# Optimization experiments

Measured on AMD Instinct MI355X. Metric: run time of the kernel, lower is better.

The kernel has to match this reference:

```python
import jax, jax.numpy as jnp
import numpy as np

D = 1024          # d_model
EXPAND = 2
DI = EXPAND * D   # d_inner = 2048
K = 4             # d_conv
B, L = 4, 2048
EPS = 1e-6


def setup_inputs() -> dict:
    key = jax.random.key(0)
    ks = jax.random.split(key, 16)
    n = lambda i, shape, scale=0.02: (jax.random.normal(ks[i], shape, jnp.float32) * scale)
    return {
        "x": jax.random.normal(ks[0], (B, L, D), jnp.float32),
        "norm_w": jnp.ones((D,), jnp.float32),
        "up_w": n(1, (D, DI)), "up_b": jnp.zeros((DI,), jnp.float32),
        "gate_w": n(2, (D, DI)), "gate_b": jnp.zeros((DI,), jnp.float32),
        "down_w": n(3, (DI, D)), "down_b": jnp.zeros((D,), jnp.float32),
        "conv_w": n(4, (DI, K), 0.2), "conv_b": jnp.zeros((DI,), jnp.float32),
        "wq": n(5, (D, D)), "wk": n(6, (D, D)), "wv": n(7, (D, D)), "wo": n(8, (D, D)),
        "decay": jnp.float32(0.99),
    }


def _rmsnorm(x, w):
    return x * jax.lax.rsqrt(jnp.mean(x * x, axis=-1, keepdims=True) + EPS) * w


def _forward(x, norm_w, up_w, up_b, gate_w, gate_b, down_w, down_b,
             conv_w, conv_b, wq, wk, wv, wo, decay):
    normed = _rmsnorm(x, norm_w)                              # [B,L,D]
    h = normed @ up_w + up_b                                  # [B,L,DI]
    # causal depthwise conv1d: left-pad K-1, groups = DI
    di = conv_w.shape[0]
    kern = conv_w.T[:, None, :]                               # [K,1,DI] (WIO)
    h = jax.lax.conv_general_dilated(
        h, kern, window_strides=(1,), padding=[(conv_w.shape[1] - 1, 0)],
        dimension_numbers=("NWC", "WIO", "NWC"), feature_group_count=di)
    h = jax.nn.silu(h + conv_b)                               # [B,L,DI]
    # gated MLP combine + down-projection
    out = (h * jax.nn.silu(normed @ gate_w + gate_b)) @ down_w + down_b  # [B,L,D]
    # Hebbian associative memory: M_t = decay*M_{t-1} + k_t^T v_t; y_t = q_t M_t
    q = out @ wq; k = out @ wk; v = out @ wv                  # [B,L,D]
    M0 = jnp.zeros((out.shape[0], out.shape[-1], out.shape[-1]), out.dtype)

    def step(M, qkv):
        qt, kt, vt = qkv                                      # each [B,D]
        M = decay * M + jnp.einsum("bd,be->bde", kt, vt)
        return M, jnp.einsum("bd,bde->be", qt, M)

    _, ys = jax.lax.scan(step, M0, (q.swapaxes(0, 1), k.swapaxes(0, 1), v.swapaxes(0, 1)))
    mem_out = ys.swapaxes(0, 1) @ wo                          # [B,L,D]
    return x + mem_out


def reference(x, norm_w, up_w, up_b, gate_w, gate_b, down_w, down_b,
              conv_w, conv_b, wq, wk, wv, wo, decay):
    return _forward(x, norm_w, up_w, up_b, gate_w, gate_b, down_w, down_b,
                    conv_w, conv_b, wq, wk, wv, wo, decay)
```

## Files before the change

### kernel.cpp

```cpp
#include <hip/hip_runtime.h>


typedef __bf16 bf16x8 __attribute__((ext_vector_type(8)));
typedef unsigned short u16x8 __attribute__((ext_vector_type(8)));
typedef float f32x4 __attribute__((ext_vector_type(4)));

constexpr int Bb = 4, Ll = 2048, Dd = 1024, DIc = 2048;
constexpr long LD  = (long)Ll * Dd;
constexpr long BLD = (long)Bb * LD;

static __device__ __forceinline__ unsigned short f2bf(float f) {
  unsigned u = __builtin_bit_cast(unsigned, f);
  u += 0x7fffu + ((u >> 16) & 1u);
  return (unsigned short)(u >> 16);
}
static __device__ __forceinline__ float bf2f(unsigned short u) {
  return __builtin_bit_cast(float, (unsigned)u << 16);
}
static __device__ __forceinline__ float silu(float g) {
  return g / (1.f + __expf(-g));
}

enum { EP_UG = 0, EP_DOWN, EP_GV, EP_DECAY, EP_YO };

#define STAGE_A(DBUF, MG, KH, TILE) {                                          \
    const int kt_ = ((TILE) < NTm1 ? (TILE) : NTm1);                           \
    __builtin_amdgcn_global_load_lds(                                          \
      (const __attribute__((address_space(1))) void*)                          \
        (Ag + (size_t)(aRow + (MG)*64) * lda + kt_*64 + (KH)*32 + aCol),       \
      (__attribute__((address_space(3))) void*)                                \
        (lds + (DBUF)*ADB + (KH)*AKH + (aRb + (MG)*4)*512), 16, 0, 0); }

#define STAGE_B(DBUF, NH, KH, TILE) {                                          \
    const int kt_ = ((TILE) < NTm1 ? (TILE) : NTm1);                           \
    __builtin_amdgcn_global_load_lds(                                          \
      (const __attribute__((address_space(1))) void*)                          \
        (Bg + (size_t)(bRow + (NH)*128) * ldb + kt_*64 + (KH)*32 + aCol),      \
      (__attribute__((address_space(3))) void*)                                \
        (lds + BOFF + (DBUF)*16384 + (KH)*8192 + ((NH)*8 + w)*512), 16, 0, 0); }

#define LOAD_A(DBUF, KS, MG) {                                                 \
  _Pragma("unroll") for (int j_ = 0; j_ < 4; ++j_)                             \
    af[j_] = *(const bf16x8*)&lds[(DBUF)*ADB + (KS)*AKH +                      \
        (aRdBase + (MG)*4 + j_)*512 + fr*32 + cph]; }

#define LOAD_B(DBUF, KS) {                                                     \
  _Pragma("unroll") for (int n_ = 0; n_ < 4; ++n_)                             \
    bfr[KS][n_] = *(const bf16x8*)&lds[BOFF + (DBUF)*16384 + (KS)*8192 +       \
        (bRb + n_)*512 + fr*32 + cph]; }

#define MFMA_PH(KS, MG) {                                                      \
  __builtin_amdgcn_s_setprio(1);                                               \
  _Pragma("unroll") for (int j_ = 0; j_ < 4; ++j_)                             \
  _Pragma("unroll") for (int n_ = 0; n_ < 4; ++n_)                             \
    acc[(MG)*4 + j_][n_] = __builtin_amdgcn_mfma_f32_16x16x32_bf16(            \
        af[j_], bfr[KS][n_], acc[(MG)*4 + j_][n_], 0, 0, 0);                   \
  __builtin_amdgcn_s_setprio(0); }

#define BAR() __builtin_amdgcn_s_barrier()
#define WAIT_LGKM0() { asm volatile("s_waitcnt lgkmcnt(0)" ::: "memory");      \
                       __builtin_amdgcn_sched_barrier(0); }
#define WAIT_LGKM8() asm volatile("s_waitcnt lgkmcnt(8)" ::: "memory")
#define WAIT_VM(N) asm volatile("s_waitcnt vmcnt(" #N ")" ::: "memory")

template <int EPI, int BM>
__global__ __launch_bounds__(512, 2) void gemm8_k(
    const ushort* __restrict__ A, const ushort* __restrict__ Bm,
    void* __restrict__ O0, const float* __restrict__ bias,
    const float* __restrict__ bias2, const float* __restrict__ xres,
    const float* __restrict__ decayp,
    int K, int lda, int ldb, int ldc,
    long sA, long sB, long sC,
    void* __restrict__ O1) {
  constexpr int MF = BM / 32;
  constexpr int ADB = BM * 64;
  constexpr int AKH = BM * 32;
  constexpr int BOFF = BM * 128;
  __shared__ ushort lds[BM == 256 ? 65536 : 49152];

  const int z = blockIdx.z;
  const int gx = gridDim.x;
  const int nwg = gx * gridDim.y;
  const int id = blockIdx.y * gx + blockIdx.x;
  const int chunk = nwg >> 3;
  const int swz = (id & 7) * chunk + (id >> 3);
  const int m0 = (swz / gx) * BM;
  const int n0 = (swz % gx) * 256;

  const int t = threadIdx.x;
  const int lane = t & 63;
  const int w = t >> 6;

  if constexpr (EPI == EP_DECAY) {
    if (n0 > m0) return;
  }
  const ushort* Ag = A + (size_t)z * sA + (size_t)m0 * lda;
  const ushort* Bg = Bm + (size_t)z * sB + (size_t)n0 * ldb;

  int Kend = K;
  if constexpr (EPI == EP_YO) Kend = (K < m0 + BM) ? K : m0 + BM;
  const int NT = Kend >> 6;
  const int NTm1 = NT - 1;
  const int NI = NT >> 1;

  const int lp = lane ^ (((lane >> 5) & 1) << 1);
  const int aCol = (lp & 3) * 8;
  const int bRow = (w >> 2) * 64 + (w & 3) * 16 + (lp >> 2);
  int aRow, aRb, aRdBase;
  if constexpr (BM == 256) {
    aRow = (w >> 2) * 128 + (w & 3) * 16 + (lp >> 2);
    aRb = (w >> 2) * 8 + (w & 3);
    aRdBase = (w >> 2) * 8;
  } else {
    aRow = w * 16 + (lp >> 2);
    aRb = w;
    aRdBase = (w >> 2) * 4;
  }
  const int fr = lane & 15;
  const int kg = (lane >> 4) * 8;
  const int cph = kg ^ (((fr >> 3) & 1) << 4);
  const int bRb = ((w & 3) >> 1) * 8 + ((w & 3) & 1) * 4;

  f32x4 acc[MF][4] = {};
  bf16x8 af[4], bfr[2][4];

  if constexpr (BM == 256) {
    STAGE_A(0, 0, 0, 0); STAGE_A(0, 0, 1, 0); STAGE_A(0, 1, 0, 0); STAGE_A(0, 1, 1, 0);
    STAGE_B(0, 0, 0, 0); STAGE_B(0, 0, 1, 0); STAGE_B(0, 1, 0, 0); STAGE_B(0, 1, 1, 0);
    STAGE_B(1, 0, 0, 1); STAGE_B(1, 0, 1, 1); STAGE_B(1, 1, 0, 1); STAGE_B(1, 1, 1, 1);
    STAGE_A(1, 0, 0, 1); STAGE_A(1, 0, 1, 1);
    WAIT_VM(6);
    BAR();
    for (int i = 0; i < NI; ++i) {
      const int tt = 2 * i;
      LOAD_B(0, 0); LOAD_B(0, 1); LOAD_A(0, 0, 0);
      STAGE_A(1, 1, 0, tt + 1); STAGE_A(1, 1, 1, tt + 1);
      WAIT_LGKM8();
      BAR(); WAIT_LGKM0();
      MFMA_PH(0, 0);
      BAR();
      LOAD_A(0, 0, 1);
      STAGE_B(0, 0, 0, tt + 2); STAGE_B(0, 1, 0, tt + 2);
      BAR(); WAIT_LGKM0();
      MFMA_PH(0, 1);
      BAR();
      LOAD_A(0, 1, 0);
      STAGE_B(0, 0, 1, tt + 2); STAGE_B(0, 1, 1, tt + 2);
      BAR(); WAIT_LGKM0();
      MFMA_PH(1, 0);
      BAR();
      LOAD_A(0, 1, 1);
      STAGE_A(0, 0, 0, tt + 2); STAGE_A(0, 0, 1, tt + 2);
      WAIT_VM(6);
      BAR(); WAIT_LGKM0();
      MFMA_PH(1, 1);
      BAR();
      LOAD_B(1, 0); LOAD_B(1, 1); LOAD_A(1, 0, 0);
      STAGE_A(0, 1, 0, tt + 2); STAGE_A(0, 1, 1, tt + 2);
      WAIT_LGKM8();
      BAR(); WAIT_LGKM0();
      MFMA_PH(0, 0);
      BAR();
      LOAD_A(1, 0, 1);
      STAGE_B(1, 0, 0, tt + 3); STAGE_B(1, 1, 0, tt + 3);
      BAR(); WAIT_LGKM0();
      MFMA_PH(0, 1);
      BAR();
      LOAD_A(1, 1, 0);
      STAGE_B(1, 0, 1, tt + 3); STAGE_B(1, 1, 1, tt + 3);
      BAR(); WAIT_LGKM0();
      MFMA_PH(1, 0);
      BAR();
      LOAD_A(1, 1, 1);
      STAGE_A(1, 0, 0, tt + 3); STAGE_A(1, 0, 1, tt + 3);
      WAIT_VM(6);
      BAR(); WAIT_LGKM0();
      MFMA_PH(1, 1);
      BAR();
    }
  } else {
    STAGE_A(0, 0, 0, 0); STAGE_A(0, 0, 1, 0);
    STAGE_B(0, 0, 0, 0); STAGE_B(0, 1, 0, 0); STAGE_B(0, 0, 1, 0); STAGE_B(0, 1, 1, 0);
    STAGE_B(1, 0, 0, 1); STAGE_B(1, 1, 0, 1); STAGE_B(1, 0, 1, 1); STAGE_B(1, 1, 1, 1);
    WAIT_VM(4);
    BAR();
    for (int i = 0; i < NI; ++i) {
      const int tt = 2 * i;
      LOAD_B(0, 0); LOAD_B(0, 1); LOAD_A(0, 0, 0);
      STAGE_A(1, 0, 0, tt + 1); STAGE_A(1, 0, 1, tt + 1);
      WAIT_LGKM8();
      BAR(); WAIT_LGKM0();
      MFMA_PH(0, 0);
      BAR();
      LOAD_A(0, 1, 0);
      STAGE_B(0, 0, 0, tt + 2); STAGE_B(0, 1, 0, tt + 2);
      STAGE_B(0, 0, 1, tt + 2); STAGE_B(0, 1, 1, tt + 2);
      WAIT_VM(4);
      BAR(); WAIT_LGKM0();
      MFMA_PH(1, 0);
      BAR();
      LOAD_B(1, 0); LOAD_B(1, 1); LOAD_A(1, 0, 0);
      STAGE_A(0, 0, 0, tt + 2); STAGE_A(0, 0, 1, tt + 2);
      WAIT_LGKM8();
      BAR(); WAIT_LGKM0();
      MFMA_PH(0, 0);
      BAR();
      LOAD_A(1, 1, 0);
      STAGE_B(1, 0, 0, tt + 3); STAGE_B(1, 1, 0, tt + 3);
      STAGE_B(1, 0, 1, tt + 3); STAGE_B(1, 1, 1, tt + 3);
      WAIT_VM(4);
      BAR(); WAIT_LGKM0();
      MFMA_PH(1, 0);
      BAR();
    }
  }

  const int rb4 = (lane >> 4) * 4;
  const int wm = (w >> 2) * (BM / 2), wn = (w & 3) * 64;
  float logd = 0.f;
  if constexpr (EPI == EP_DECAY) logd = __logf(decayp[0]);

#pragma unroll
  for (int mf = 0; mf < MF; ++mf) {
#pragma unroll
    for (int nf = 0; nf < 4; ++nf) {
      const int gm0 = m0 + wm + mf * 16 + rb4;
      const int gn = n0 + wn + nf * 16 + fr;
      if constexpr (EPI == EP_GV) {
        if (gn < 1024) {
#pragma unroll
          for (int r = 0; r < 4; ++r)
            ((ushort*)O0)[(size_t)(gm0 + r) * 1024 + gn] = f2bf(acc[mf][nf][r]);
        } else {
          const int d = gn - 1024, b = gm0 >> 11, ttp = gm0 & 2047;
          ushort4 w4;
          w4.x = f2bf(acc[mf][nf][0]); w4.y = f2bf(acc[mf][nf][1]);
          w4.z = f2bf(acc[mf][nf][2]); w4.w = f2bf(acc[mf][nf][3]);
          *(ushort4*)&((ushort*)O1)[(size_t)b * LD + (size_t)d * Ll + ttp] = w4;
        }
      } else {
#pragma unroll
        for (int r = 0; r < 4; ++r) {
          const int gm = gm0 + r;
          const size_t idx = (size_t)z * sC + (size_t)gm * ldc + gn;
          const float v = acc[mf][nf][r];
          if constexpr (EPI == EP_UG) {
            const float b = (gn < 2048) ? bias[gn] : bias2[gn - 2048];
            ((ushort*)O0)[idx] = f2bf(v + b);
          } else if constexpr (EPI == EP_DOWN) {
            ((ushort*)O0)[idx] = f2bf(v + bias[gn]);
          } else if constexpr (EPI == EP_DECAY) {
            ((ushort*)O0)[idx] =
                (gn <= gm) ? f2bf(v * __expf((float)(gm - gn) * logd)) : (ushort)0;
          } else {
            ((float*)O0)[idx] = v + xres[idx];
          }
        }
      }
    }
  }
}

__global__ __launch_bounds__(256) void prep_k(
    const float* __restrict__ up_w, const float* __restrict__ gate_w,
    const float* __restrict__ down_w, const float* __restrict__ wq,
    const float* __restrict__ wk, const float* __restrict__ wv,
    const float* __restrict__ wo, const float* __restrict__ conv_w,
    const float* __restrict__ x, const float* __restrict__ norm_w,
    ushort* __restrict__ ugw, ushort* __restrict__ down_wT,
    ushort* __restrict__ wq_bf, ushort* __restrict__ wk_bf,
    ushort* __restrict__ wv_bf, ushort* __restrict__ wo_T,
    ushort* __restrict__ cwT, ushort* __restrict__ nrm) {
  const int bid = blockIdx.x;
  const int t = threadIdx.x;
  if (bid < 7168) {
    const float* src; ushort* dst; int R, C, idx;
    if (bid < 2048)      { src = up_w;   dst = ugw;               R = 1024; C = 2048; idx = bid; }
    else if (bid < 4096) { src = gate_w; dst = ugw + 2048 * 1024; R = 1024; C = 2048; idx = bid - 2048; }
    else if (bid < 6144) { src = down_w; dst = down_wT;           R = 2048; C = 1024; idx = bid - 4096; }
    else                 { src = wo;     dst = wo_T;              R = 1024; C = 1024; idx = bid - 6144; }
    __shared__ float tile[32][33];
    const int tx = t & 31, ty = t >> 5;
    const int tilesx = C >> 5;
    const int c0 = (idx % tilesx) * 32, r0 = (idx / tilesx) * 32;
#pragma unroll
    for (int i = 0; i < 4; ++i)
      tile[ty + i * 8][tx] = src[(size_t)(r0 + ty + i * 8) * C + c0 + tx];
    __syncthreads();
#pragma unroll
    for (int i = 0; i < 4; ++i)
      dst[(size_t)(c0 + ty + i * 8) * R + r0 + tx] = f2bf(tile[tx][ty + i * 8]);
  } else if (bid < 10240) {
    const int seg = (bid - 7168) >> 10;
    const int idx = (bid - 7168) & 1023;
    const float* src = (seg == 0) ? wq : (seg == 1) ? wk : wv;
    ushort* dst = (seg == 0) ? wq_bf : (seg == 1) ? wk_bf : wv_bf;
    const size_t e = (size_t)idx * 1024 + t * 4;
    const float4 v = *(const float4*)(src + e);
    ushort4 r;
    r.x = f2bf(v.x); r.y = f2bf(v.y); r.z = f2bf(v.z); r.w = f2bf(v.w);
    *(ushort4*)(dst + e) = r;
  } else if (bid < 10248) {
    const int c = (bid - 10240) * 256 + t;
    const float4 v = *(const float4*)(conv_w + c * 4);
    cwT[0 * DIc + c] = f2bf(v.x);
    cwT[1 * DIc + c] = f2bf(v.y);
    cwT[2 * DIc + c] = f2bf(v.z);
    cwT[3 * DIc + c] = f2bf(v.w);
  } else {
    const int row = bid - 10248;
    const float* xr = x + (size_t)row * Dd;
    const float4 v = *(const float4*)(xr + t * 4);
    float ss = v.x * v.x + v.y * v.y + v.z * v.z + v.w * v.w;
#pragma unroll
    for (int m = 32; m; m >>= 1) ss += __shfl_xor(ss, m);
    __shared__ float red[4];
    if ((t & 63) == 0) red[t >> 6] = ss;
    __syncthreads();
    const float total = red[0] + red[1] + red[2] + red[3];
    const float rs = rsqrtf(total * (1.f / (float)Dd) + 1e-6f);
    const float4 wt = *(const float4*)(norm_w + t * 4);
    ushort4 r;
    r.x = f2bf(v.x * rs * wt.x); r.y = f2bf(v.y * rs * wt.y);
    r.z = f2bf(v.z * rs * wt.z); r.w = f2bf(v.w * rs * wt.w);
    *(ushort4*)(nrm + (size_t)row * Dd + t * 4) = r;
  }
}

__global__ __launch_bounds__(256) void conv_gate_k(
    const ushort* __restrict__ ug, const ushort* __restrict__ cwT,
    const float* __restrict__ cb, ushort* __restrict__ o,
    const ushort* __restrict__ wk_bf, const ushort* __restrict__ wq_bf,
    const ushort* __restrict__ wo_T, const ushort* __restrict__ wv_bf,
    ushort* __restrict__ WsT, ushort* __restrict__ Wv2T) {
  const int bid = blockIdx.x;
  const int t = threadIdx.x;
  if (bid < 128) {
    __shared__ ushort lds[8192];
    ushort* As = lds;
    ushort* Bs = lds + 4096;
    const int oo = bid >> 6, lid = bid & 63;
    const int m0 = (lid >> 3) * 128, n0 = (lid & 7) * 128;
    const ushort* A = (oo ? wo_T : wk_bf) + (size_t)m0 * 1024;
    const ushort* B = (oo ? wv_bf : wq_bf) + (size_t)n0 * 1024;
    ushort* C = oo ? Wv2T : WsT;
    const int lane = t & 63, wave = t >> 6;
    const int wm = (wave >> 1) * 64, wn = (wave & 1) * 64;
    const int fr = lane & 15, kg = (lane >> 4) * 8;
    const int srow0 = wave * 16 + (lane >> 2), scol = (lane & 3) * 8;
    f32x4 acc[4][4] = {};
    for (int k0 = 0; k0 < 1024; k0 += 32) {
#pragma unroll
      for (int p = 0; p < 2; ++p) {
        __builtin_amdgcn_global_load_lds(
            (const __attribute__((address_space(1))) void*)
                (A + (size_t)(srow0 + p * 64) * 1024 + k0 + scol),
            (__attribute__((address_space(3))) void*)(As + (p * 4 + wave) * 512),
            16, 0, 0);
        __builtin_amdgcn_global_load_lds(
            (const __attribute__((address_space(1))) void*)
                (B + (size_t)(srow0 + p * 64) * 1024 + k0 + scol),
            (__attribute__((address_space(3))) void*)(Bs + (p * 4 + wave) * 512),
            16, 0, 0);
      }
      __syncthreads();
      bf16x8 af[4], bv[4];
#pragma unroll
      for (int i = 0; i < 4; ++i) {
        af[i] = *(const bf16x8*)&As[(wm + i * 16 + fr) * 32 + kg];
        bv[i] = *(const bf16x8*)&Bs[(wn + i * 16 + fr) * 32 + kg];
      }
#pragma unroll
      for (int mi = 0; mi < 4; ++mi)
#pragma unroll
        for (int ni = 0; ni < 4; ++ni)
          acc[mi][ni] = __builtin_amdgcn_mfma_f32_16x16x32_bf16(
              af[mi], bv[ni], acc[mi][ni], 0, 0, 0);
      __syncthreads();
    }
    const int rb = (lane >> 4) * 4;
#pragma unroll
    for (int mi = 0; mi < 4; ++mi)
#pragma unroll
      for (int ni = 0; ni < 4; ++ni)
#pragma unroll
        for (int r = 0; r < 4; ++r)
          C[(size_t)(m0 + wm + mi * 16 + rb + r) * 1024 + n0 + wn + ni * 16 + fr] =
              f2bf(acc[mi][ni][r]);
    return;
  }

  const int cbid = bid - 128;
  const int cg = t & 31;
  const int ts = t >> 5;
  const int cblk = cbid & 7;
  const int rblk = cbid >> 3;
  const int c = cblk * 256 + cg * 8;
  const int row0 = rblk * 64 + ts * 8;

  u16x8 w[4];
#pragma unroll
  for (int k = 0; k < 4; ++k) w[k] = *(const u16x8*)&cwT[k * DIc + c];
  float wb[8];
  *(float4*)&wb[0] = *(const float4*)(cb + c);
  *(float4*)&wb[4] = *(const float4*)(cb + c + 4);

  u16x8 h3, h2, h1;
  if ((row0 & (Ll - 1)) == 0) {
    h3 = (u16x8){}; h2 = (u16x8){}; h1 = (u16x8){};
  } else {
    h3 = *(const u16x8*)&ug[(size_t)(row0 - 3) * 4096 + c];
    h2 = *(const u16x8*)&ug[(size_t)(row0 - 2) * 4096 + c];
    h1 = *(const u16x8*)&ug[(size_t)(row0 - 1) * 4096 + c];
  }

#pragma unroll
  for (int i = 0; i < 8; ++i) {
    const size_t rbase = (size_t)(row0 + i) * 4096;
    const u16x8 h0 = *(const u16x8*)&ug[rbase + c];
    const u16x8 g  = *(const u16x8*)&ug[rbase + 2048 + c];
    u16x8 ov;
#pragma unroll
    for (int j = 0; j < 8; ++j) {
      float acc = wb[j];
      acc += bf2f(w[0][j]) * bf2f(h3[j]);
      acc += bf2f(w[1][j]) * bf2f(h2[j]);
      acc += bf2f(w[2][j]) * bf2f(h1[j]);
      acc += bf2f(w[3][j]) * bf2f(h0[j]);
      ov[j] = f2bf(silu(acc) * silu(bf2f(g[j])));
    }
    *(u16x8*)&o[(size_t)(row0 + i) * DIc + c] = ov;
    h3 = h2; h2 = h1; h1 = h0;
  }
}

extern "C" void kernel_launch(void* const* d_in, const int* in_sizes, int n_in,
                              void* d_out, int out_size, void* d_ws,
                              size_t ws_size, hipStream_t stream) {
  const float* x      = (const float*)d_in[0];
  const float* norm_w = (const float*)d_in[1];
  const float* up_w   = (const float*)d_in[2];
  const float* up_b   = (const float*)d_in[3];
  const float* gate_w = (const float*)d_in[4];
  const float* gate_b = (const float*)d_in[5];
  const float* down_w = (const float*)d_in[6];
  const float* down_b = (const float*)d_in[7];
  const float* conv_w = (const float*)d_in[8];
  const float* conv_b = (const float*)d_in[9];
  const float* wq     = (const float*)d_in[10];
  const float* wk     = (const float*)d_in[11];
  const float* wv     = (const float*)d_in[12];
  const float* wo     = (const float*)d_in[13];
  const float* decay  = (const float*)d_in[14];
  float* out = (float*)d_out;
  char* w8 = (char*)d_ws;

  const size_t MiB = 1u << 20;
  ushort* nrm      = (ushort*)(w8 + 0 * MiB);
  ushort* ug       = (ushort*)(w8 + 16 * MiB);
  ushort* S        = (ushort*)(w8 + 16 * MiB);
  ushort* combined = (ushort*)(w8 + 80 * MiB);
  ushort* G        = (ushort*)(w8 + 112 * MiB);
  ushort* vT       = (ushort*)(w8 + 144 * MiB);
  ushort* ugw      = (ushort*)(w8 + 176 * MiB);
  ushort* down_wT  = (ushort*)(w8 + 184 * MiB);
  ushort* wq_bf    = (ushort*)(w8 + 188 * MiB);
  ushort* wk_bf    = (ushort*)(w8 + 190 * MiB);
  ushort* wv_bf    = (ushort*)(w8 + 192 * MiB);
  ushort* wo_T     = (ushort*)(w8 + 194 * MiB);
  ushort* WsT      = (ushort*)(w8 + 196 * MiB);
  ushort* Wv2T     = (ushort*)(w8 + 198 * MiB);
  ushort* cwT      = (ushort*)(w8 + 200 * MiB);

  prep_k<<<18440, 256, 0, stream>>>(up_w, gate_w, down_w, wq, wk, wv, wo,
                                    conv_w, x, norm_w,
                                    ugw, down_wT, wq_bf, wk_bf, wv_bf, wo_T,
                                    cwT, nrm);

  gemm8_k<EP_UG, 256><<<dim3(16, 32), 512, 0, stream>>>(
      nrm, ugw, ug, up_b, gate_b, nullptr, nullptr,
      1024, 1024, 1024, 4096, 0, 0, 0, nullptr);

  conv_gate_k<<<1152, 256, 0, stream>>>(ug, cwT, conv_b, combined,
                                        wk_bf, wq_bf, wo_T, wv_bf, WsT, Wv2T);

  gemm8_k<EP_DOWN, 128><<<dim3(4, 64), 512, 0, stream>>>(
      combined, down_wT, nrm, down_b, nullptr, nullptr, nullptr,
      2048, 2048, 2048, 1024, 0, 0, 0, nullptr);

  gemm8_k<EP_GV, 128><<<dim3(8, 64), 512, 0, stream>>>(
      nrm, WsT, G, nullptr, nullptr, nullptr, nullptr,
      1024, 1024, 1024, 1024, 0, 0, 0, vT);

  gemm8_k<EP_DECAY, 256><<<dim3(8, 8, Bb), 512, 0, stream>>>(
      G, nrm, S, nullptr, nullptr, nullptr, decay,
      1024, 1024, 1024, 2048, LD, LD, (long)Ll * Ll, nullptr);

  gemm8_k<EP_YO, 128><<<dim3(4, 16, Bb), 512, 0, stream>>>(
      S, vT, out, nullptr, nullptr, x, nullptr,
      2048, 2048, 2048, 1024, (long)Ll * Ll, LD, LD, nullptr);
}
```

Baseline: 280.5 us.

## Add 128x128 GEMM kernel for causal decay and output GEMMs with balanced scheduling

Adds a new 256-thread 128x128-tile GEMM kernel, which now runs the causal decay-score GEMM and the output GEMM that was previously done by the 512-thread 256/128-row kernel. With finer tiles the triangular masking skips more of the zero upper-triangle work. The output GEMM pairs short and long causal row tiles so workgroups get balanced K lengths. The GV GEMM also switches to 256-row tiles. More, smaller workgroups reduce operand reuse per tile.

```diff
diff --git a/kernel.cpp b/kernel.cpp
--- a/kernel.cpp
+++ b/kernel.cpp
@@ -67,8 +67,7 @@
 __global__ __launch_bounds__(512, 2) void gemm8_k(
     const ushort* __restrict__ A, const ushort* __restrict__ Bm,
     void* __restrict__ O0, const float* __restrict__ bias,
-    const float* __restrict__ bias2, const float* __restrict__ xres,
-    const float* __restrict__ decayp,
+    const float* __restrict__ bias2,
     int K, int lda, int ldb, int ldc,
     long sA, long sB, long sC,
     void* __restrict__ O1) {
@@ -91,15 +90,10 @@
   const int lane = t & 63;
   const int w = t >> 6;
 
-  if constexpr (EPI == EP_DECAY) {
-    if (n0 > m0) return;
-  }
   const ushort* Ag = A + (size_t)z * sA + (size_t)m0 * lda;
   const ushort* Bg = Bm + (size_t)z * sB + (size_t)n0 * ldb;
 
-  int Kend = K;
-  if constexpr (EPI == EP_YO) Kend = (K < m0 + BM) ? K : m0 + BM;
-  const int NT = Kend >> 6;
+  const int NT = K >> 6;
   const int NTm1 = NT - 1;
   const int NI = NT >> 1;
 
@@ -217,8 +211,6 @@
 
   const int rb4 = (lane >> 4) * 4;
   const int wm = (w >> 2) * (BM / 2), wn = (w & 3) * 64;
-  float logd = 0.f;
-  if constexpr (EPI == EP_DECAY) logd = __logf(decayp[0]);
 
 #pragma unroll
   for (int mf = 0; mf < MF; ++mf) {
@@ -247,14 +239,164 @@
           if constexpr (EPI == EP_UG) {
             const float b = (gn < 2048) ? bias[gn] : bias2[gn - 2048];
             ((ushort*)O0)[idx] = f2bf(v + b);
-          } else if constexpr (EPI == EP_DOWN) {
+          } else {
             ((ushort*)O0)[idx] = f2bf(v + bias[gn]);
-          } else if constexpr (EPI == EP_DECAY) {
-            ((ushort*)O0)[idx] =
-                (gn <= gm) ? f2bf(v * __expf((float)(gm - gn) * logd)) : (ushort)0;
-          } else {
-            ((float*)O0)[idx] = v + xres[idx];
           }
+        }
+      }
+    }
+  }
+}
+
+#define S4A(DBUF, MG, KH, TILE) {                                              \
+    const int kt_ = ((TILE) < NTm1 ? (TILE) : NTm1);                           \
+    __builtin_amdgcn_global_load_lds(                                          \
+      (const __attribute__((address_space(1))) void*)                          \
+        (Ag + (size_t)(sRow + (MG)*64) * lda + kt_*64 + (KH)*32 + sCol),       \
+      (__attribute__((address_space(3))) void*)                                \
+        (lds + (DBUF)*8192 + (KH)*4096 + ((MG)*4 + w4)*512), 16, 0, 0); }
+
+#define S4B(DBUF, NH, KH, TILE) {                                              \
+    const int kt_ = ((TILE) < NTm1 ? (TILE) : NTm1);                           \
+    __builtin_amdgcn_global_load_lds(                                          \
+      (const __attribute__((address_space(1))) void*)                          \
+        (Bg + (size_t)(sRow + (NH)*64) * ldb + kt_*64 + (KH)*32 + sCol),       \
+      (__attribute__((address_space(3))) void*)                                \
+        (lds + 16384 + (DBUF)*8192 + (KH)*4096 + ((NH)*4 + w4)*512), 16, 0, 0); }
+
+#define L4A(DBUF, KS) {                                                        \
+  _Pragma("unroll") for (int j_ = 0; j_ < 4; ++j_)                             \
+    af[j_] = *(const bf16x8*)&lds[(DBUF)*8192 + (KS)*4096 +                    \
+        (aRd + j_)*512 + fr*32 + cph]; }
+
+#define L4B(DBUF, KS) {                                                        \
+  _Pragma("unroll") for (int n_ = 0; n_ < 4; ++n_)                             \
+    bfr[KS][n_] = *(const bf16x8*)&lds[16384 + (DBUF)*8192 + (KS)*4096 +       \
+        (bRd + n_)*512 + fr*32 + cph]; }
+
+#define MFMA4(KS) {                                                            \
+  __builtin_amdgcn_s_setprio(1);                                               \
+  _Pragma("unroll") for (int j_ = 0; j_ < 4; ++j_)                             \
+  _Pragma("unroll") for (int n_ = 0; n_ < 4; ++n_)                             \
+    acc[j_][n_] = __builtin_amdgcn_mfma_f32_16x16x32_bf16(                     \
+        af[j_], bfr[KS][n_], acc[j_][n_], 0, 0, 0);                            \
+  __builtin_amdgcn_s_setprio(0); }
+
+template <int EPI>
+__global__ __launch_bounds__(256, 2) void gemm4_k(
+    const ushort* __restrict__ A, const ushort* __restrict__ Bm,
+    void* __restrict__ O0, const float* __restrict__ xres,
+    const float* __restrict__ decayp,
+    int K, int lda, int ldb, int ldc, long sA, long sB, long sC) {
+  __shared__ ushort lds[32768];
+
+  const int t = threadIdx.x;
+  const int lane = t & 63;
+  const int w4 = t >> 6;
+
+  int z, m0, n0;
+  if constexpr (EPI == EP_YO) {
+    const int id = blockIdx.y * gridDim.x + blockIdx.x;
+    const int half = id >> 8;
+    const int u = id & 255;
+    const int nt = u & 7;
+    const int rem = u >> 3;
+    z = rem >> 3;
+    const int i8 = rem & 7;
+    const int mt = half ? (15 - i8) : i8;
+    m0 = mt * 128;
+    n0 = nt * 128;
+  } else {
+    z = blockIdx.z;
+    const int gx = gridDim.x;
+    const int nwg = gx * gridDim.y;
+    const int id = blockIdx.y * gx + blockIdx.x;
+    const int chunk = nwg >> 3;
+    const int swz = (id & 7) * chunk + (id >> 3);
+    m0 = (swz / gx) * 128;
+    n0 = (swz % gx) * 128;
+    if (n0 > m0) return;
+  }
+
+  const ushort* Ag = A + (size_t)z * sA + (size_t)m0 * lda;
+  const ushort* Bg = Bm + (size_t)z * sB + (size_t)n0 * ldb;
+
+  int Kend = K;
+  if constexpr (EPI == EP_YO) Kend = m0 + 128;
+  const int NT = Kend >> 6;
+  const int NTm1 = NT - 1;
+  const int NI = NT >> 1;
+
+  const int lp = lane ^ (((lane >> 5) & 1) << 1);
+  const int sRow = w4 * 16 + (lp >> 2);
+  const int sCol = (lp & 3) * 8;
+  const int fr = lane & 15;
+  const int kg = (lane >> 4) * 8;
+  const int cph = kg ^ (((fr >> 3) & 1) << 4);
+  const int aRd = (w4 >> 1) * 4;
+  const int bRd = (w4 & 1) * 4;
+
+  f32x4 acc[4][4] = {};
+  bf16x8 af[4], bfr[2][4];
+
+  S4A(0, 0, 0, 0); S4A(0, 1, 0, 0); S4A(0, 0, 1, 0); S4A(0, 1, 1, 0);
+  S4B(0, 0, 0, 0); S4B(0, 1, 0, 0); S4B(0, 0, 1, 0); S4B(0, 1, 1, 0);
+  S4B(1, 0, 0, 1); S4B(1, 1, 0, 1); S4B(1, 0, 1, 1); S4B(1, 1, 1, 1);
+  WAIT_VM(4);
+  BAR();
+  for (int i = 0; i < NI; ++i) {
+    const int tt = 2 * i;
+    L4B(0, 0); L4B(0, 1); L4A(0, 0);
+    S4A(1, 0, 0, tt + 1); S4A(1, 1, 0, tt + 1);
+    S4A(1, 0, 1, tt + 1); S4A(1, 1, 1, tt + 1);
+    WAIT_LGKM8();
+    BAR(); WAIT_LGKM0();
+    MFMA4(0);
+    BAR();
+    L4A(0, 1);
+    S4B(0, 0, 0, tt + 2); S4B(0, 1, 0, tt + 2);
+    S4B(0, 0, 1, tt + 2); S4B(0, 1, 1, tt + 2);
+    WAIT_VM(4);
+    BAR(); WAIT_LGKM0();
+    MFMA4(1);
+    BAR();
+    L4B(1, 0); L4B(1, 1); L4A(1, 0);
+    S4A(0, 0, 0, tt + 2); S4A(0, 1, 0, tt + 2);
+    S4A(0, 0, 1, tt + 2); S4A(0, 1, 1, tt + 2);
+    WAIT_LGKM8();
+    BAR(); WAIT_LGKM0();
+    MFMA4(0);
+    BAR();
+    L4A(1, 1);
+    S4B(1, 0, 0, tt + 3); S4B(1, 1, 0, tt + 3);
+    S4B(1, 0, 1, tt + 3); S4B(1, 1, 1, tt + 3);
+    WAIT_VM(4);
+    BAR(); WAIT_LGKM0();
+    MFMA4(1);
+    BAR();
+  }
+
+  const int rb4 = (lane >> 4) * 4;
+  const int wm = (w4 >> 1) * 64, wn = (w4 & 1) * 64;
+  float logd = 0.f;
+  if constexpr (EPI == EP_DECAY) logd = __logf(decayp[0]);
+
+#pragma unroll
+  for (int mf = 0; mf < 4; ++mf) {
+#pragma unroll
+    for (int nf = 0; nf < 4; ++nf) {
+      const int gm0 = m0 + wm + mf * 16 + rb4;
+      const int gn = n0 + wn + nf * 16 + fr;
+#pragma unroll
+      for (int r = 0; r < 4; ++r) {
+        const int gm = gm0 + r;
+        const size_t idx = (size_t)z * sC + (size_t)gm * ldc + gn;
+        const float v = acc[mf][nf][r];
+        if constexpr (EPI == EP_DECAY) {
+          ((ushort*)O0)[idx] =
+              (gn <= gm) ? f2bf(v * __expf((float)(gm - gn) * logd)) : (ushort)0;
+        } else {
+          ((float*)O0)[idx] = v + xres[idx];
         }
       }
     }
@@ -478,25 +620,25 @@
                                     cwT, nrm);
 
   gemm8_k<EP_UG, 256><<<dim3(16, 32), 512, 0, stream>>>(
-      nrm, ugw, ug, up_b, gate_b, nullptr, nullptr,
+      nrm, ugw, ug, up_b, gate_b,
       1024, 1024, 1024, 4096, 0, 0, 0, nullptr);
 
   conv_gate_k<<<1152, 256, 0, stream>>>(ug, cwT, conv_b, combined,
                                         wk_bf, wq_bf, wo_T, wv_bf, WsT, Wv2T);
 
   gemm8_k<EP_DOWN, 128><<<dim3(4, 64), 512, 0, stream>>>(
-      combined, down_wT, nrm, down_b, nullptr, nullptr, nullptr,
+      combined, down_wT, nrm, down_b, nullptr,
       2048, 2048, 2048, 1024, 0, 0, 0, nullptr);
 
-  gemm8_k<EP_GV, 128><<<dim3(8, 64), 512, 0, stream>>>(
-      nrm, WsT, G, nullptr, nullptr, nullptr, nullptr,
+  gemm8_k<EP_GV, 256><<<dim3(8, 32), 512, 0, stream>>>(
+      nrm, WsT, G, nullptr, nullptr,
       1024, 1024, 1024, 1024, 0, 0, 0, vT);
 
-  gemm8_k<EP_DECAY, 256><<<dim3(8, 8, Bb), 512, 0, stream>>>(
-      G, nrm, S, nullptr, nullptr, nullptr, decay,
-      1024, 1024, 1024, 2048, LD, LD, (long)Ll * Ll, nullptr);
-
-  gemm8_k<EP_YO, 128><<<dim3(4, 16, Bb), 512, 0, stream>>>(
-      S, vT, out, nullptr, nullptr, x, nullptr,
-      2048, 2048, 2048, 1024, (long)Ll * Ll, LD, LD, nullptr);
-}
+  gemm4_k<EP_DECAY><<<dim3(16, 16, Bb), 256, 0, stream>>>(
+      G, nrm, S, nullptr, decay,
+      1024, 1024, 1024, 2048, LD, LD, (long)Ll * Ll);
+
+  gemm4_k<EP_YO><<<dim3(8, 64), 256, 0, stream>>>(
+      S, vT, out, x, nullptr,
+      0, 2048, 2048, 1024, (long)Ll * Ll, LD, LD);
+}
```

Result: faster. 273.7 us (-2.4%).
